# Optimization experiments

Hardware: AMD Instinct MI355X
Metric: run time of the kernel (lower is better)

The kernel has to match this reference:

```python
import jax, jax.numpy as jnp
import numpy as np

N, H, W, C = 16, 160, 160, 80          # images, feature HxW, classes (A=1)
STRIDE, ANCHOR = 8, 64
IMG = H * STRIDE                        # image size 1280
PRE_THRESH = 0.05                       # pre_nms_thresh
PRE_K = 1000                            # pre_nms_top_n
NMS_THR = 0.8                           # nms_thresh_test (eval mode)
POST_K = 200                            # post_nms_topk_test (eval mode)
MIN_SIZE = 0.0
WX, WY, WW, WH = 10.0, 10.0, 5.0, 5.0   # ATSS BoxCoder weights
BBOX_XFORM_CLIP = float(np.log(1000.0 / 16.0))


def setup_inputs() -> dict:
    key = jax.random.key(0)
    k1, k2, k3 = jax.random.split(key, 3)
    # logits shifted down so only ~a realistic fraction pass the 0.05 threshold
    box_cls = jax.random.normal(k1, (N, C, H, W), jnp.float32) - 4.0
    box_regression = jax.random.normal(k2, (N, 4, H, W), jnp.float32)
    centerness = jax.random.normal(k3, (N, 1, H, W), jnp.float32)
    ys, xs = np.meshgrid(np.arange(H), np.arange(W), indexing="ij")
    cx = (xs.reshape(-1) + 0.5) * STRIDE
    cy = (ys.reshape(-1) + 0.5) * STRIDE
    half = ANCHOR / 2.0
    anchors = jnp.asarray(
        np.stack([cx - half, cy - half, cx + half, cy + half], 1), jnp.float32)
    return {"box_cls": box_cls, "box_regression": box_regression,
            "centerness": centerness, "anchors": anchors}


def _decode(deltas, anchors):
    widths = anchors[:, 2] - anchors[:, 0] + 1.0
    heights = anchors[:, 3] - anchors[:, 1] + 1.0
    ctr_x = anchors[:, 0] + 0.5 * widths
    ctr_y = anchors[:, 1] + 0.5 * heights
    dx = deltas[:, 0] / WX
    dy = deltas[:, 1] / WY
    dw = jnp.minimum(deltas[:, 2] / WW, BBOX_XFORM_CLIP)
    dh = jnp.minimum(deltas[:, 3] / WH, BBOX_XFORM_CLIP)
    pcx = dx * widths + ctr_x
    pcy = dy * heights + ctr_y
    pw = jnp.exp(dw) * widths
    ph = jnp.exp(dh) * heights
    return jnp.stack([pcx - 0.5 * pw, pcy - 0.5 * ph,
                      pcx + 0.5 * pw - 1.0, pcy + 0.5 * ph - 1.0], 1)


def _iou_row(box, boxes):
    x1 = jnp.maximum(box[0], boxes[:, 0])
    y1 = jnp.maximum(box[1], boxes[:, 1])
    x2 = jnp.minimum(box[2], boxes[:, 2])
    y2 = jnp.minimum(box[3], boxes[:, 3])
    inter = jnp.maximum(x2 - x1, 0.0) * jnp.maximum(y2 - y1, 0.0)
    a1 = jnp.maximum(box[2] - box[0], 0.0) * jnp.maximum(box[3] - box[1], 0.0)
    a2 = jnp.maximum(boxes[:, 2] - boxes[:, 0], 0.0) * jnp.maximum(boxes[:, 3] - boxes[:, 1], 0.0)
    return inter / jnp.maximum(a1 + a2 - inter, 1e-9)


def _per_image(cls_logits, reg, ctr_logits, anchors):
    # cls_logits [HWA,C], reg [HWA,4], ctr_logits [HWA], anchors [HWA,4]
    probs = jax.nn.sigmoid(cls_logits)
    cand = probs > PRE_THRESH
    n_cand = jnp.minimum(cand.sum(), PRE_K)            # pre_nms_top_n.clamp
    scores = probs * jax.nn.sigmoid(ctr_logits)[:, None]
    masked = jnp.where(cand, scores, -1.0).reshape(-1)  # [HWA*C]
    topv, topi = jax.lax.top_k(masked, PRE_K)           # fixed-size topk over candidates
    valid = (topv > 0.0) & (jnp.arange(PRE_K) < n_cand)
    loc = topi // C
    labels = (topi % C + 1).astype(jnp.float32)
    boxes = _decode(reg[loc], anchors[loc])
    boxes = jnp.clip(boxes, 0.0, IMG - 1.0)              # clip_to_image
    ws = boxes[:, 2] - boxes[:, 0] + 1.0
    hs = boxes[:, 3] - boxes[:, 1] + 1.0
    valid = valid & (ws >= MIN_SIZE) & (hs >= MIN_SIZE)  # remove_small_boxes
    det_scores = jnp.where(valid, jnp.sqrt(jnp.maximum(topv, 0.0)), 0.0)
    # sort by score desc, then class-aware greedy NMS
    sv, order = jax.lax.top_k(det_scores, PRE_K)
    boxes_s = boxes[order]
    off = labels[order] * (IMG + 1.0)                    # ml_nms class offset
    nb = boxes_s + off[:, None]
    keep0 = sv > 0.0
    idx = jnp.arange(PRE_K)
    def body(i, keep):
        iou = _iou_row(nb[i], nb)
        sup = (iou > NMS_THR) & (idx > i) & keep[i]
        return keep & ~sup
    keep = jax.lax.fori_loop(0, PRE_K, body, keep0)
    final = jnp.where(keep, sv, 0.0)
    fv, fi = jax.lax.top_k(final, POST_K)                # post_nms_topk (kthvalue filter)
    out_boxes = jnp.where(fv[:, None] > 0.0, boxes_s[fi], 0.0)
    return jnp.concatenate([out_boxes, fv[:, None]], 1)  # [POST_K, 5]


def reference(box_cls, box_regression, centerness, anchors):
    # permute_and_flatten: [N, A*C, H, W] -> [N, H*W*A, C] (A=1)
    cls = box_cls.transpose(0, 2, 3, 1).reshape(N, H * W, C)
    reg = box_regression.transpose(0, 2, 3, 1).reshape(N, H * W, 4)
    ctr = centerness.transpose(0, 2, 3, 1).reshape(N, H * W)
    return jax.vmap(_per_image, in_axes=(0, 0, 0, None))(cls, reg, ctr, anchors)
```

## Files before the change

### kernel.cpp

```cpp
#include <hip/hip_runtime.h>
#include <stdint.h>

typedef unsigned long long u64;
typedef unsigned int u32;

#define NIMG 16
#define NC 80
#define HW 25600
#define CHW (NC * HW)
#define PREK 1000
#define POSTK 200
#define HB2 2048
#define CAPLDS 4096
#define CANDCAP 131072
#define STAGE_CAP 2048
#define EPB 16384
#define LOGIT_T (-2.9444389791664403f)
#define SFLOOR 0.05f
#define CLIPDWH 4.135166556742356f
#define IMGM1 1279.0f
#define OFFMUL 1281.0f
#define NMSTHR 0.8f

__global__ __launch_bounds__(256) void k_scan(const float* __restrict__ cls,
                                              const float* __restrict__ ctr,
                                              int* __restrict__ gcount,
                                              u64* __restrict__ cand) {
  __shared__ u64 stg[STAGE_CAP];
  __shared__ int scnt, sbase;
  const int n = blockIdx.y, tid = threadIdx.x, lane = tid & 63;
  if (tid == 0) scnt = 0;
  __syncthreads();
  const float* ctrRow = ctr + (size_t)n * HW;
  const size_t base = (size_t)n * CHW + (size_t)blockIdx.x * EPB;
  for (int it = 0; it < 16; ++it) {
    const int e0 = it * 1024 + tid * 4;
    const float4 v = *reinterpret_cast<const float4*>(cls + base + e0);
    const float L[4] = {v.x, v.y, v.z, v.w};
#pragma unroll
    for (int u = 0; u < 4; ++u) {
      const int e = blockIdx.x * EPB + e0 + u;
      float s = -1.0f;
      bool pass = false;
      u64 pk = 0;
      if (L[u] > LOGIT_T) {
        float p  = 1.0f / (1.0f + expf(-L[u]));
        int loc = e % HW;
        float cg = 1.0f / (1.0f + expf(-ctrRow[loc]));
        s = p * cg;
        if (s > SFLOOR) {
          int c = e / HW;
          u32 idx = (u32)(loc * NC + c);
          pk = ((u64)__float_as_uint(s) << 32) | (u32)(~idx);
          pass = true;
        }
      }
      u64 m = __ballot(pass);
      if (m) {
        int leader = __ffsll(m) - 1;
        int basew = 0;
        if (lane == leader) basew = atomicAdd(&scnt, __popcll(m));
        basew = __shfl(basew, leader);
        if (pass) {
          int pos = basew + __popcll(m & ((1ULL << lane) - 1ULL));
          if (pos < STAGE_CAP) stg[pos] = pk;
          else {
            int gp = atomicAdd(&gcount[n], 1);
            if (gp < CANDCAP) cand[(size_t)n * CANDCAP + gp] = pk;
          }
        }
      }
    }
  }
  __syncthreads();
  if (tid == 0) {
    int c = scnt < STAGE_CAP ? scnt : STAGE_CAP;
    sbase = atomicAdd(&gcount[n], c);
  }
  __syncthreads();
  int c = scnt < STAGE_CAP ? scnt : STAGE_CAP;
  for (int i = tid; i < c; i += 256) {
    int gp = sbase + i;
    if (gp < CANDCAP) cand[(size_t)n * CANDCAP + gp] = stg[i];
  }
}

__global__ __launch_bounds__(1024) void k_selsort(const u64* __restrict__ cand,
                                                  const int* __restrict__ gcount,
                                                  u64* __restrict__ top,
                                                  int* __restrict__ gnc) {
  __shared__ u64 a[CAPLDS];
  __shared__ int hh[HB2];
  __shared__ int ss[1024];
  __shared__ int sB, selK;
  const int n = blockIdx.x, t = threadIdx.x, lane = t & 63;
  int cnt = gcount[n]; if (cnt > CANDCAP) cnt = CANDCAP;
  for (int i = t; i < HB2; i += 1024) hh[i] = 0;
  for (int i = t; i < CAPLDS; i += 1024) a[i] = 0ULL;
  if (t == 0) { selK = 0; sB = HB2; }
  __syncthreads();
  const u64* C = cand + (size_t)n * CANDCAP;
  for (int i = t; i < cnt; i += 1024)
    atomicAdd(&hh[(u32)(C[i] >> 51)], 1);
  __syncthreads();
  ss[t] = hh[2 * t] + hh[2 * t + 1];
  __syncthreads();
  for (int off = 1; off < 1024; off <<= 1) {
    int v = (t + off < 1024) ? ss[t + off] : 0;
    __syncthreads();
    ss[t] += v;
    __syncthreads();
  }
  const int total = ss[0];
  const int ncand = total < PREK ? total : PREK;
  if (t == 0) gnc[n] = ncand;
  if (total > 0) {
    int Sn = (t < 1023) ? ss[t + 1] : 0;
    if (ss[t] >= ncand && Sn < ncand) {
      int run = Sn, B = 2 * t;
      for (int b = 2 * t + 1; b >= 2 * t; --b) {
        run += hh[b];
        if (run >= ncand) { B = b; break; }
      }
      sB = B;
    }
  }
  __syncthreads();
  const u32 B = (u32)sB;
  const int cntR = (cnt + 1023) & ~1023;
  for (int i = t; i < cntR; i += 1024) {
    bool pass = false; u64 pk = 0;
    if (i < cnt) { pk = C[i]; pass = ((u32)(pk >> 51) >= B); }
    u64 m = __ballot(pass);
    if (m) {
      int leader = __ffsll(m) - 1;
      int basew = 0;
      if (lane == leader) basew = atomicAdd(&selK, __popcll(m));
      basew = __shfl(basew, leader);
      if (pass) {
        int pos = basew + __popcll(m & ((1ULL << lane) - 1ULL));
        if (pos < CAPLDS) a[pos] = pk;
      }
    }
  }
  __syncthreads();
  for (int k = 2; k <= CAPLDS; k <<= 1)
    for (int j = k >> 1; j > 0; j >>= 1) {
      for (int i = t; i < CAPLDS; i += 1024) {
        int ix = i ^ j;
        if (ix > i) {
          u64 x = a[i], y = a[ix];
          bool desc = ((i & k) == 0);
          if (desc ? (x < y) : (x > y)) { a[i] = y; a[ix] = x; }
        }
      }
      __syncthreads();
    }
  if (t < 1024) top[(size_t)n * 1024 + t] = a[t];
}

__global__ void k_decode(const u64* __restrict__ top, const int* __restrict__ gnc,
                         const float* __restrict__ reg, const float* __restrict__ anch,
                         float4* __restrict__ boxes, float4* __restrict__ nb,
                         float* __restrict__ dsc) {
  const int n = blockIdx.x, k = threadIdx.x;
  if (k >= PREK) return;
  u64 pk = top[(size_t)n * 1024 + k];
  int ncand = gnc[n];
  float4 bx = {0, 0, 0, 0}, nbv = {0, 0, 0, 0};
  float d = 0.0f;
  if (k < ncand && pk != 0ULL) {
    float s = __uint_as_float((u32)(pk >> 32));
    u32 idx = ~(u32)pk;
    int loc = idx / NC, c = idx - loc * NC;
    float r0 = reg[((size_t)n * 4 + 0) * HW + loc];
    float r1 = reg[((size_t)n * 4 + 1) * HW + loc];
    float r2 = reg[((size_t)n * 4 + 2) * HW + loc];
    float r3 = reg[((size_t)n * 4 + 3) * HW + loc];
    float a0 = anch[loc * 4 + 0], a1 = anch[loc * 4 + 1];
    float a2 = anch[loc * 4 + 2], a3 = anch[loc * 4 + 3];
    float w = a2 - a0 + 1.0f, h = a3 - a1 + 1.0f;
    float cx = a0 + 0.5f * w, cy = a1 + 0.5f * h;
    float dx = r0 / 10.0f, dy = r1 / 10.0f;
    float dw = fminf(r2 / 5.0f, CLIPDWH), dh = fminf(r3 / 5.0f, CLIPDWH);
    float pcx = dx * w + cx, pcy = dy * h + cy;
    float pw = expf(dw) * w, ph = expf(dh) * h;
    float x1 = pcx - 0.5f * pw, y1 = pcy - 0.5f * ph;
    float x2 = pcx + 0.5f * pw - 1.0f, y2 = pcy + 0.5f * ph - 1.0f;
    x1 = fminf(fmaxf(x1, 0.0f), IMGM1); y1 = fminf(fmaxf(y1, 0.0f), IMGM1);
    x2 = fminf(fmaxf(x2, 0.0f), IMGM1); y2 = fminf(fmaxf(y2, 0.0f), IMGM1);
    float wsz = x2 - x1 + 1.0f, hsz = y2 - y1 + 1.0f;
    if (wsz >= 0.0f && hsz >= 0.0f) d = sqrtf(s);
    bx = {x1, y1, x2, y2};
    float off = (float)(c + 1) * OFFMUL;
    nbv = {x1 + off, y1 + off, x2 + off, y2 + off};
  }
  boxes[n * PREK + k] = bx;
  nb[n * PREK + k] = nbv;
  dsc[n * PREK + k] = d;
}

__global__ void k_sup(const float4* __restrict__ nb, const float* __restrict__ dsc,
                      u64* __restrict__ sup) {
  const int i = blockIdx.x, n = blockIdx.y;
  if (dsc[n * PREK + i] == 0.0f) return;
  const float4 bi = nb[n * PREK + i];
  const float a1 = fmaxf(bi.z - bi.x, 0.0f) * fmaxf(bi.w - bi.y, 0.0f);
  const int tid = threadIdx.x, lane = tid & 63, wv = tid >> 6;
#pragma unroll
  for (int rep = 0; rep < 4; ++rep) {
    int j = rep * 256 + tid;
    bool bit = false;
    if (j < PREK && j > i) {
      float4 bj = nb[n * PREK + j];
      float xx1 = fmaxf(bi.x, bj.x), yy1 = fmaxf(bi.y, bj.y);
      float xx2 = fminf(bi.z, bj.z), yy2 = fminf(bi.w, bj.w);
      float inter = fmaxf(xx2 - xx1, 0.0f) * fmaxf(yy2 - yy1, 0.0f);
      float a2 = fmaxf(bj.z - bj.x, 0.0f) * fmaxf(bj.w - bj.y, 0.0f);
      float iou = inter / fmaxf(a1 + a2 - inter, 1e-9f);
      bit = iou > NMSTHR;
    }
    u64 m = __ballot(bit);
    if (lane == 0) sup[((size_t)n * PREK + i) * 16 + rep * 4 + wv] = m;
  }
}

__global__ void k_greedy(const float* __restrict__ dsc, const float4* __restrict__ boxes,
                         const u64* __restrict__ sup, float* __restrict__ out) {
  const int n = blockIdx.x;
  const int lane = threadIdx.x;
  const float* d = dsc + n * PREK;
  u64 keep0 = 0;
  for (int w = 0; w < 16; ++w) {
    int i = w * 64 + lane;
    bool b = (i < PREK) && (d[i] > 0.0f);
    u64 m = __ballot(b);
    if (lane == w) keep0 = m;
  }
  const u64* S = sup + (size_t)n * PREK * 16;
  u64 removed = 0;
#define LDR(r) ((lane < 16 && (r) < PREK) ? S[(size_t)(r) * 16 + lane] : 0ULL)
  u64 p0 = LDR(0), p1 = LDR(1), p2 = LDR(2), p3 = LDR(3);
  u64 p4 = LDR(4), p5 = LDR(5), p6 = LDR(6), p7 = LDR(7);
#define STEP(ii, pr) { \
    u64 cur = __shfl(keep0 & ~removed, (ii) >> 6); \
    if ((cur >> ((ii) & 63)) & 1ULL) removed |= pr; \
    pr = LDR((ii) + 8); }
  for (int ib = 0; ib < PREK; ib += 8) {
    STEP(ib + 0, p0) STEP(ib + 1, p1) STEP(ib + 2, p2) STEP(ib + 3, p3)
    STEP(ib + 4, p4) STEP(ib + 5, p5) STEP(ib + 6, p6) STEP(ib + 7, p7)
  }
#undef STEP
#undef LDR
  u64 fk = keep0 & ~removed;
  int base = 0;
  for (int w = 0; w < 16; ++w) {
    u64 m = __shfl(fk, w);
    int i = w * 64 + lane;
    bool kept = (m >> lane) & 1ULL;
    int rank = base + __popcll(m & ((1ULL << lane) - 1ULL));
    if (kept && rank < POSTK && i < PREK) {
      float4 b = boxes[n * PREK + i];
      float* o = out + ((size_t)n * POSTK + rank) * 5;
      o[0] = b.x; o[1] = b.y; o[2] = b.z; o[3] = b.w; o[4] = d[i];
    }
    base += __popcll(m);
  }
}

extern "C" void kernel_launch(void* const* d_in, const int* in_sizes, int n_in,
                              void* d_out, int out_size, void* d_ws, size_t ws_size,
                              hipStream_t stream) {
  (void)in_sizes; (void)n_in; (void)ws_size;
  const float* cls  = (const float*)d_in[0];
  const float* reg  = (const float*)d_in[1];
  const float* ctr  = (const float*)d_in[2];
  const float* anch = (const float*)d_in[3];
  float* out = (float*)d_out;
  char* ws = (char*)d_ws;

  int*    gcount = (int*)(ws + 0);
  int*    gnc    = (int*)(ws + 64);
  u64*    cand   = (u64*)(ws + 128);
  u64*    top    = (u64*)(ws + 16777344);
  float4* boxes  = (float4*)(ws + 16908416);
  float4* nb     = (float4*)(ws + 17164416);
  float*  dsc    = (float*)(ws + 17420416);
  u64*    sup    = (u64*)(ws + 17484416);

  hipMemsetAsync(ws, 0, 128, stream);
  hipMemsetAsync(d_out, 0, (size_t)out_size * sizeof(float), stream);

  dim3 gScan(CHW / EPB, NIMG);
  k_scan   <<<gScan, 256, 0, stream>>>(cls, ctr, gcount, cand);
  k_selsort<<<NIMG, 1024, 0, stream>>>(cand, gcount, top, gnc);
  k_decode <<<NIMG, 1024, 0, stream>>>(top, gnc, reg, anch, boxes, nb, dsc);
  dim3 gSup(PREK, NIMG);
  k_sup    <<<gSup, 256, 0, stream>>>(nb, dsc, sup);
  k_greedy <<<NIMG, 64, 0, stream>>>(dsc, boxes, sup, out);
}
```

Baseline: 495.0 us.

## Fuse decode and NMS into one kernel using per-class bucketed greedy NMS

Replaces the decode, the full 1000x1000 suppression-mask kernel and the serial greedy kernel with a single per-image kernel. Candidates are bucketed by class in LDS, and each wavefront runs greedy NMS within a class, since the class offset keeps boxes of different classes from overlapping. This avoids the global sup matrix, two kernel launches and the 1000-step serial scan. In exchange it adds a serial per-class bucketing loop and caps each class at 128 candidates, which could drop boxes if one class exceeds that.

```diff
diff --git a/kernel.cpp b/kernel.cpp
--- a/kernel.cpp
+++ b/kernel.cpp
@@ -15,6 +15,7 @@
 #define CANDCAP 131072
 #define STAGE_CAP 2048
 #define EPB 16384
+#define CCAP 128
 #define LOGIT_T (-2.9444389791664403f)
 #define SFLOOR 0.05f
 #define CLIPDWH 4.135166556742356f
@@ -40,14 +41,13 @@
 #pragma unroll
     for (int u = 0; u < 4; ++u) {
       const int e = blockIdx.x * EPB + e0 + u;
-      float s = -1.0f;
       bool pass = false;
       u64 pk = 0;
       if (L[u] > LOGIT_T) {
         float p  = 1.0f / (1.0f + expf(-L[u]));
         int loc = e % HW;
         float cg = 1.0f / (1.0f + expf(-ctrRow[loc]));
-        s = p * cg;
+        float s = p * cg;
         if (s > SFLOOR) {
           int c = e / HW;
           u32 idx = (u32)(loc * NC + c);
@@ -159,20 +159,39 @@
   if (t < 1024) top[(size_t)n * 1024 + t] = a[t];
 }
 
-__global__ void k_decode(const u64* __restrict__ top, const int* __restrict__ gnc,
-                         const float* __restrict__ reg, const float* __restrict__ anch,
-                         float4* __restrict__ boxes, float4* __restrict__ nb,
-                         float* __restrict__ dsc) {
-  const int n = blockIdx.x, k = threadIdx.x;
-  if (k >= PREK) return;
-  u64 pk = top[(size_t)n * 1024 + k];
-  int ncand = gnc[n];
+__device__ __forceinline__ bool iou_gt(float4 a, float4 b) {
+  float x1 = fmaxf(a.x, b.x), y1 = fmaxf(a.y, b.y);
+  float x2 = fminf(a.z, b.z), y2 = fminf(a.w, b.w);
+  float inter = fmaxf(x2 - x1, 0.0f) * fmaxf(y2 - y1, 0.0f);
+  float a1 = fmaxf(a.z - a.x, 0.0f) * fmaxf(a.w - a.y, 0.0f);
+  float a2 = fmaxf(b.z - b.x, 0.0f) * fmaxf(b.w - b.y, 0.0f);
+  return inter / fmaxf(a1 + a2 - inter, 1e-9f) > NMSTHR;
+}
+
+__global__ __launch_bounds__(1024) void k_nms(const u64* __restrict__ top,
+                                              const int* __restrict__ gnc,
+                                              const float* __restrict__ reg,
+                                              const float* __restrict__ anch,
+                                              float4* __restrict__ boxScr,
+                                              float* __restrict__ out) {
+  __shared__ float4 nbL[1024];
+  __shared__ float dL[1024];
+  __shared__ unsigned char clsL[1024];
+  __shared__ unsigned short ord[NC * CCAP];
+  __shared__ int ccnt[NC];
+  __shared__ unsigned short keptIdx[16 * CCAP];
+  __shared__ unsigned char keptFlag[1024];
+  __shared__ int ss[1024];
+  const int n = blockIdx.x, t = threadIdx.x, lane = t & 63, wv = t >> 6;
+  const int ncand = gnc[n];
+  u64 pk = top[(size_t)n * 1024 + t];
   float4 bx = {0, 0, 0, 0}, nbv = {0, 0, 0, 0};
   float d = 0.0f;
-  if (k < ncand && pk != 0ULL) {
+  int c = 0;
+  if (t < PREK && t < ncand && pk != 0ULL) {
     float s = __uint_as_float((u32)(pk >> 32));
     u32 idx = ~(u32)pk;
-    int loc = idx / NC, c = idx - loc * NC;
+    int loc = idx / NC; c = idx - loc * NC;
     float r0 = reg[((size_t)n * 4 + 0) * HW + loc];
     float r1 = reg[((size_t)n * 4 + 1) * HW + loc];
     float r2 = reg[((size_t)n * 4 + 2) * HW + loc];
@@ -195,76 +214,73 @@
     float off = (float)(c + 1) * OFFMUL;
     nbv = {x1 + off, y1 + off, x2 + off, y2 + off};
   }
-  boxes[n * PREK + k] = bx;
-  nb[n * PREK + k] = nbv;
-  dsc[n * PREK + k] = d;
-}
-
-__global__ void k_sup(const float4* __restrict__ nb, const float* __restrict__ dsc,
-                      u64* __restrict__ sup) {
-  const int i = blockIdx.x, n = blockIdx.y;
-  if (dsc[n * PREK + i] == 0.0f) return;
-  const float4 bi = nb[n * PREK + i];
-  const float a1 = fmaxf(bi.z - bi.x, 0.0f) * fmaxf(bi.w - bi.y, 0.0f);
-  const int tid = threadIdx.x, lane = tid & 63, wv = tid >> 6;
-#pragma unroll
-  for (int rep = 0; rep < 4; ++rep) {
-    int j = rep * 256 + tid;
-    bool bit = false;
-    if (j < PREK && j > i) {
-      float4 bj = nb[n * PREK + j];
-      float xx1 = fmaxf(bi.x, bj.x), yy1 = fmaxf(bi.y, bj.y);
-      float xx2 = fminf(bi.z, bj.z), yy2 = fminf(bi.w, bj.w);
-      float inter = fmaxf(xx2 - xx1, 0.0f) * fmaxf(yy2 - yy1, 0.0f);
-      float a2 = fmaxf(bj.z - bj.x, 0.0f) * fmaxf(bj.w - bj.y, 0.0f);
-      float iou = inter / fmaxf(a1 + a2 - inter, 1e-9f);
-      bit = iou > NMSTHR;
-    }
-    u64 m = __ballot(bit);
-    if (lane == 0) sup[((size_t)n * PREK + i) * 16 + rep * 4 + wv] = m;
-  }
-}
-
-__global__ void k_greedy(const float* __restrict__ dsc, const float4* __restrict__ boxes,
-                         const u64* __restrict__ sup, float* __restrict__ out) {
-  const int n = blockIdx.x;
-  const int lane = threadIdx.x;
-  const float* d = dsc + n * PREK;
-  u64 keep0 = 0;
-  for (int w = 0; w < 16; ++w) {
-    int i = w * 64 + lane;
-    bool b = (i < PREK) && (d[i] > 0.0f);
-    u64 m = __ballot(b);
-    if (lane == w) keep0 = m;
-  }
-  const u64* S = sup + (size_t)n * PREK * 16;
-  u64 removed = 0;
-#define LDR(r) ((lane < 16 && (r) < PREK) ? S[(size_t)(r) * 16 + lane] : 0ULL)
-  u64 p0 = LDR(0), p1 = LDR(1), p2 = LDR(2), p3 = LDR(3);
-  u64 p4 = LDR(4), p5 = LDR(5), p6 = LDR(6), p7 = LDR(7);
-#define STEP(ii, pr) { \
-    u64 cur = __shfl(keep0 & ~removed, (ii) >> 6); \
-    if ((cur >> ((ii) & 63)) & 1ULL) removed |= pr; \
-    pr = LDR((ii) + 8); }
-  for (int ib = 0; ib < PREK; ib += 8) {
-    STEP(ib + 0, p0) STEP(ib + 1, p1) STEP(ib + 2, p2) STEP(ib + 3, p3)
-    STEP(ib + 4, p4) STEP(ib + 5, p5) STEP(ib + 6, p6) STEP(ib + 7, p7)
-  }
-#undef STEP
-#undef LDR
-  u64 fk = keep0 & ~removed;
-  int base = 0;
-  for (int w = 0; w < 16; ++w) {
-    u64 m = __shfl(fk, w);
-    int i = w * 64 + lane;
-    bool kept = (m >> lane) & 1ULL;
-    int rank = base + __popcll(m & ((1ULL << lane) - 1ULL));
-    if (kept && rank < POSTK && i < PREK) {
-      float4 b = boxes[n * PREK + i];
+  nbL[t] = nbv; dL[t] = d; clsL[t] = (unsigned char)c; keptFlag[t] = 0;
+  if (t < PREK) boxScr[n * PREK + t] = bx;
+  if (t < NC) ccnt[t] = 0;
+  __syncthreads();
+  if (t < NC) {
+    int pos = 0;
+    for (int k = 0; k < PREK; ++k)
+      if (dL[k] > 0.0f && clsL[k] == (unsigned char)t) {
+        if (pos < CCAP) ord[t * CCAP + pos] = (unsigned short)k;
+        ++pos;
+      }
+    ccnt[t] = pos < CCAP ? pos : CCAP;
+  }
+  __syncthreads();
+  for (int cc = wv; cc < NC; cc += 16) {
+    const int ncls = ccnt[cc];
+    if (ncls == 0) continue;
+    int nkept = 0;
+    for (int s0 = 0; s0 < ncls; s0 += 64) {
+      const int j = s0 + lane;
+      const bool inr = j < ncls;
+      const int myk = inr ? ord[cc * CCAP + j] : 0;
+      const float4 mb = nbL[myk];
+      bool dead = false;
+      for (int tt = 0; tt < nkept; ++tt)
+        dead |= iou_gt(nbL[keptIdx[wv * CCAP + tt]], mb);
+      const int lim = (ncls - s0) < 64 ? (ncls - s0) : 64;
+      u64 supby = 0;
+      for (int i = 0; i < lim; ++i) {
+        bool sgt = iou_gt(nbL[ord[cc * CCAP + s0 + i]], mb);
+        if (i < lane) supby |= (u64)sgt << i;
+      }
+      u64 live = __ballot(inr && !dead);
+      u64 keptm = 0;
+      while (true) {
+        u64 rem = live & ~keptm;
+        if (!rem) break;
+        int i = __ffsll(rem) - 1;
+        keptm |= 1ULL << i;
+        u64 supped = __ballot((supby >> i) & 1ULL);
+        live &= ~(supped & ~((2ULL << i) - 1ULL));
+      }
+      int myrank = nkept + __popcll(keptm & ((1ULL << lane) - 1ULL));
+      if ((keptm >> lane) & 1ULL) {
+        keptIdx[wv * CCAP + myrank] = (unsigned short)myk;
+        keptFlag[myk] = 1;
+      }
+      nkept += __popcll(keptm);
+    }
+  }
+  __syncthreads();
+  const int flag = keptFlag[t];
+  ss[t] = flag;
+  __syncthreads();
+  for (int off = 1; off < 1024; off <<= 1) {
+    int v = (t >= off) ? ss[t - off] : 0;
+    __syncthreads();
+    ss[t] += v;
+    __syncthreads();
+  }
+  if (flag) {
+    int rank = ss[t] - 1;
+    if (rank < POSTK) {
+      float4 b = boxScr[n * PREK + t];
       float* o = out + ((size_t)n * POSTK + rank) * 5;
-      o[0] = b.x; o[1] = b.y; o[2] = b.z; o[3] = b.w; o[4] = d[i];
-    }
-    base += __popcll(m);
+      o[0] = b.x; o[1] = b.y; o[2] = b.z; o[3] = b.w; o[4] = dL[t];
+    }
   }
 }
 
@@ -283,10 +299,7 @@
   int*    gnc    = (int*)(ws + 64);
   u64*    cand   = (u64*)(ws + 128);
   u64*    top    = (u64*)(ws + 16777344);
-  float4* boxes  = (float4*)(ws + 16908416);
-  float4* nb     = (float4*)(ws + 17164416);
-  float*  dsc    = (float*)(ws + 17420416);
-  u64*    sup    = (u64*)(ws + 17484416);
+  float4* boxScr = (float4*)(ws + 16908416);
 
   hipMemsetAsync(ws, 0, 128, stream);
   hipMemsetAsync(d_out, 0, (size_t)out_size * sizeof(float), stream);
@@ -294,8 +307,5 @@
   dim3 gScan(CHW / EPB, NIMG);
   k_scan   <<<gScan, 256, 0, stream>>>(cls, ctr, gcount, cand);
   k_selsort<<<NIMG, 1024, 0, stream>>>(cand, gcount, top, gnc);
-  k_decode <<<NIMG, 1024, 0, stream>>>(top, gnc, reg, anch, boxes, nb, dsc);
-  dim3 gSup(PREK, NIMG);
-  k_sup    <<<gSup, 256, 0, stream>>>(nb, dsc, sup);
-  k_greedy <<<NIMG, 64, 0, stream>>>(dsc, boxes, sup, out);
-}
+  k_nms    <<<NIMG, 1024, 0, stream>>>(top, gnc, reg, anch, boxScr, out);
+}
```

Result: no change. 502.1 us (+1.4%).
